# Kernel optimization log

Measured on AMD Instinct MI355X. Metric: run time of the kernel, lower is better.

Reference implementation:

```python
import jax, jax.numpy as jnp
import numpy as np

N_NODES = 100000
N_EDGES = 1600000
IN_FEATS = 512
OUT_FEATS = 256


def setup_inputs() -> dict:
    key = jax.random.key(0)
    k1, k2, k3, k4, k5 = jax.random.split(key, 5)
    feat = jax.random.normal(k1, (N_NODES, IN_FEATS), dtype=jnp.float32)
    W = jax.random.normal(k2, (OUT_FEATS, IN_FEATS), dtype=jnp.float32) * (1.0 / np.sqrt(IN_FEATS))
    b = jax.random.normal(k3, (OUT_FEATS,), dtype=jnp.float32) * 0.01
    src = jax.random.randint(k4, (N_EDGES,), 0, N_NODES, dtype=jnp.int32)
    dst = jax.random.randint(k5, (N_EDGES,), 0, N_NODES, dtype=jnp.int32)
    return {"feat": feat, "W": W, "b": b, "src": src, "dst": dst}


def reference(feat, W, b, src, dst):
    # Linear projection: h = feat @ W^T + b   -> [N, out_feats]
    h = jnp.einsum('nf,of->no', feat, W) + b
    # DGL update_all(copy_src, sum): for each edge (s, d), message = h[s],
    # reduce = sum over incoming edges at each destination node.
    # Nodes with no in-edges get zeros (DGL sum-reduce default).
    msgs = h[src]  # [E, out_feats] gather
    h_out = jax.ops.segment_sum(msgs, dst, num_segments=N_NODES)  # [N, out_feats]
    return h_out
```

## Files before the change

kernel.cpp:

```cpp
#include <hip/hip_runtime.h>
#include <hip/hip_bf16.h>
#include <stdint.h>

#define N_NODES 100000
#define IN_F    512
#define OUT_F   256
#define N_EDGES 1600000

typedef __attribute__((ext_vector_type(4))) float f32x4;
typedef __attribute__((ext_vector_type(8))) short bf16x8;
typedef __attribute__((ext_vector_type(8))) uint16_t u16x8;
typedef __attribute__((ext_vector_type(4))) uint32_t u32x4;

#define BM 128
#define BK 32
#define KT_TILES (IN_F / BK)
#define WFRAG_KT_STRIDE (16 * 16 * 32)
#define EPS 66
#define MTILES ((N_NODES + BM - 1) / BM)

#define NBUCK 391
#define BCAP  4608
#define SC_EDGES 8192
#define NBLK_SC ((N_EDGES + SC_EDGES - 1) / SC_EDGES)

__device__ __forceinline__ float bf2f(uint16_t u) {
    union { uint32_t i; float f; } c; c.i = ((uint32_t)u) << 16; return c.f;
}
__device__ __forceinline__ uint16_t f2bf(float f) {
    union { float f; uint32_t i; } c; c.f = f;
    uint32_t x = c.i;
    return (uint16_t)((x + 0x7FFFu + ((x >> 16) & 1u)) >> 16);
}
__device__ __forceinline__ uint32_t cvt_pk_bf16(float a, float b) {
    uint32_t r;
    asm("v_cvt_pk_bf16_f32 %0, %1, %2" : "=v"(r) : "v"(a), "v"(b));
    return r;
}
__device__ __forceinline__ void gload_lds16(const float* g, float* l) {
    __builtin_amdgcn_global_load_lds(
        (const __attribute__((address_space(1))) void*)g,
        (__attribute__((address_space(3))) void*)l, 16, 0, 0);
}
#define SYNC_VM(N) do {                                        \
    asm volatile("s_waitcnt vmcnt(" #N ")" ::: "memory");      \
    __builtin_amdgcn_s_barrier();                              \
} while (0)

__global__ __launch_bounds__(256) void w_frag_kernel(
    const float* __restrict__ W, uint16_t* __restrict__ w_frag)
{
    const int gid = blockIdx.x * 256 + threadIdx.x;
    if (gid >= 16384) return;
    const int kg = gid & 3, lrow = (gid >> 2) & 15, cg = (gid >> 6) & 15, kt = gid >> 10;
    const float* s = W + (size_t)(cg * 16 + lrow) * IN_F + kt * 32 + kg * 8;
    const f32x4 v0 = *(const f32x4*)s;
    const f32x4 v1 = *(const f32x4*)(s + 4);
    u32x4 c;
    c[0] = cvt_pk_bf16(v0[0], v0[1]);
    c[1] = cvt_pk_bf16(v0[2], v0[3]);
    c[2] = cvt_pk_bf16(v1[0], v1[1]);
    c[3] = cvt_pk_bf16(v1[2], v1[3]);
    *(u32x4*)(w_frag + (size_t)gid * 8) = c;
}

__global__ __launch_bounds__(512) void bucket_init_kernel(int* __restrict__ bucket_cursor)
{
    const int i = threadIdx.x;
    if (i < NBUCK) bucket_cursor[i] = i * BCAP;
}

__global__ __launch_bounds__(512) void gemm_scatter_kernel(
    const float* __restrict__ feat, const uint16_t* __restrict__ w_frag,
    const float* __restrict__ bias, uint16_t* __restrict__ h,
    const int* __restrict__ src, const int* __restrict__ dst,
    int* __restrict__ bucket_cursor, uint32_t* __restrict__ pairs)
{
    __shared__ __align__(16) char smem_raw[3 * BM * BK * 4];

    if (blockIdx.x >= MTILES) {
        int* bh    = (int*)smem_raw;
        int* bbase = bh + NBUCK;
        const int tid = threadIdx.x;
        for (int i = tid; i < NBUCK; i += 512) bh[i] = 0;
        __syncthreads();
        const int base = (int)(blockIdx.x - MTILES) * SC_EDGES;
        uint32_t pk[SC_EDGES / 512];
        int      bk[SC_EDGES / 512];
        #pragma unroll
        for (int k = 0; k < SC_EDGES / 512; ++k) {
            const int e = base + k * 512 + tid;
            if (e < N_EDGES) {
                const int d = dst[e], s = src[e];
                bk[k] = d >> 8;
                pk[k] = ((uint32_t)s << 8) | (uint32_t)(d & 255);
                atomicAdd(&bh[bk[k]], 1);
            } else {
                bk[k] = -1; pk[k] = 0;
            }
        }
        __syncthreads();
        for (int i = tid; i < NBUCK; i += 512) {
            const int c = bh[i];
            bbase[i] = c ? atomicAdd(&bucket_cursor[i], c) : 0;
            bh[i] = 0;
        }
        __syncthreads();
        #pragma unroll
        for (int k = 0; k < SC_EDGES / 512; ++k) {
            if (bk[k] >= 0) {
                const int r = atomicAdd(&bh[bk[k]], 1);
                pairs[bbase[bk[k]] + r] = pk[k];
            }
        }
        return;
    }

    float (*At)[BM][BK] = (float (*)[BM][BK])smem_raw;

    const int m0 = blockIdx.x * BM;

    const int t    = threadIdx.x;
    const int wid  = t >> 6;
    const int lane = t & 63;
    const int wr   = wid >> 2, wc = wid & 3;
    const int lrow = lane & 15;
    const int kg   = lane >> 4;

    f32x4 acc[4][4] = {};

    const int r8 = lane >> 3;
    const int sp = lane & 7;
    const int sc = sp ^ r8;
    const float* gsrc[2];
    #pragma unroll
    for (int i = 0; i < 2; ++i) {
        int grow = m0 + wid * 16 + i * 8 + r8;
        if (grow > N_NODES - 1) grow = N_NODES - 1;
        gsrc[i] = feat + (size_t)grow * IN_F + sc * 4;
    }

#define STAGE(KT, BUF)                                                     \
    do {                                                                   \
        gload_lds16(gsrc[0] + (KT) * BK, &At[BUF][wid * 16][0]);           \
        gload_lds16(gsrc[1] + (KT) * BK, &At[BUF][wid * 16 + 8][0]);       \
    } while (0)

    const uint16_t* wfp[4];
    #pragma unroll
    for (int n = 0; n < 4; ++n) {
        const int cg = wc * 4 + n;
        wfp[n] = w_frag + ((size_t)cg * 16 + lrow) * 32 + kg * 8;
    }

    bf16x8 bfr[2][4];

    #pragma unroll
    for (int n = 0; n < 4; ++n) bfr[0][n] = *(const bf16x8*)(wfp[n]);
    STAGE(0, 0);
    STAGE(1, 1);
    SYNC_VM(0);

    const int p0 = (2 * kg) ^ (lrow & 7);
    const int p1 = p0 ^ 1;

    #pragma unroll
    for (int kt = 0; kt < KT_TILES; ++kt) {
        const int cur = kt % 3;
        if (kt + 1 < KT_TILES) {
            #pragma unroll
            for (int n = 0; n < 4; ++n)
                bfr[(kt + 1) & 1][n] =
                    *(const bf16x8*)(wfp[n] + (size_t)(kt + 1) * WFRAG_KT_STRIDE);
        }
        if (kt + 2 < KT_TILES) STAGE(kt + 2, (kt + 2) % 3);

        bf16x8 af[4];
        #pragma unroll
        for (int m = 0; m < 4; ++m) {
            const int row = wr * 64 + m * 16 + lrow;
            const f32x4 v0 = *(const f32x4*)&At[cur][row][p0 * 4];
            const f32x4 v1 = *(const f32x4*)&At[cur][row][p1 * 4];
            union { bf16x8 v; uint32_t u[4]; } c_;
            c_.u[0] = cvt_pk_bf16(v0[0], v0[1]);
            c_.u[1] = cvt_pk_bf16(v0[2], v0[3]);
            c_.u[2] = cvt_pk_bf16(v1[0], v1[1]);
            c_.u[3] = cvt_pk_bf16(v1[2], v1[3]);
            af[m] = c_.v;
        }
        #pragma unroll
        for (int m = 0; m < 4; ++m)
            #pragma unroll
            for (int n = 0; n < 4; ++n)
                acc[m][n] = __builtin_amdgcn_mfma_f32_16x16x32_bf16(
                    af[m], bfr[kt & 1][n], acc[m][n], 0, 0, 0);

        if (kt <= KT_TILES - 3)       SYNC_VM(6);
        else if (kt == KT_TILES - 2)  SYNC_VM(4);
    }
#undef STAGE

    __syncthreads();

    uint16_t* ep = (uint16_t*)smem_raw;
    const int wbase = wid * (16 * EPS);
    float bv[4];
    #pragma unroll
    for (int n = 0; n < 4; ++n) bv[n] = bias[wc * 64 + n * 16 + lrow];

    #pragma unroll
    for (int m = 0; m < 4; ++m) {
        #pragma unroll
        for (int n = 0; n < 4; ++n)
            #pragma unroll
            for (int j = 0; j < 4; ++j)
                ep[wbase + (kg * 4 + j) * EPS + n * 16 + lrow] = f2bf(acc[m][n][j] + bv[n]);
        __syncthreads();
        #pragma unroll
        for (int g = 0; g < 4; ++g) {
            const int r16  = g * 4 + (lane >> 4);
            const int cidx = (lane & 15) * 4;
            const int ib = wbase + r16 * EPS + cidx;
            uint2 v;
            v.x = *(const uint32_t*)&ep[ib];
            v.y = *(const uint32_t*)&ep[ib + 2];
            const int row = m0 + wr * 64 + m * 16 + r16;
            if (row < N_NODES)
                *(uint2*)(h + (size_t)row * OUT_F + wc * 64 + cidx) = v;
        }
        __syncthreads();
    }
}

__global__ __launch_bounds__(256) void bucket_sort_kernel(
    const uint32_t* __restrict__ pairs, const int* __restrict__ bucket_cursor,
    int* __restrict__ start, int* __restrict__ deg, int* __restrict__ csr_src)
{
    __shared__ int hist[256];
    __shared__ int cur[256];
    __shared__ int tsum[256];
    const int b = blockIdx.x;
    const int t = threadIdx.x;
    const int ebeg = b * BCAP;
    const int eend = bucket_cursor[b];
    hist[t] = 0;
    __syncthreads();
    for (int i = ebeg + t; i < eend; i += 256)
        atomicAdd(&hist[pairs[i] & 255], 1);
    __syncthreads();
    const int c = hist[t];
    int x = c;
    tsum[t] = x; __syncthreads();
    for (int off = 1; off < 256; off <<= 1) {
        const int y = (t >= off) ? tsum[t - off] : 0;
        __syncthreads();
        x += y; tsum[t] = x;
        __syncthreads();
    }
    const int ex = x - c;
    const int node = (b << 8) + t;
    if (node < N_NODES) {
        start[node] = ebeg + ex;
        deg[node]   = c;
    }
    cur[t] = ebeg + ex;
    __syncthreads();
    for (int i = ebeg + t; i < eend; i += 256) {
        const uint32_t p = pairs[i];
        const int pos = atomicAdd(&cur[p & 255], 1);
        csr_src[pos] = (int)(p >> 8);
    }
}

__global__ __launch_bounds__(256) void gcn_gather_kernel(
    const uint16_t* __restrict__ h, const int* __restrict__ start,
    const int* __restrict__ deg, const int* __restrict__ csr_src,
    float* __restrict__ out)
{
    const int n = blockIdx.x * 4 + (threadIdx.x >> 6);
    if (n >= N_NODES) return;
    const int lane = threadIdx.x & 63;
    const int half = lane >> 5;
    const int hl   = lane & 31;
    const int beg = start[n];
    const int end = beg + deg[n];

    float a[8] = {0.f, 0.f, 0.f, 0.f, 0.f, 0.f, 0.f, 0.f};

    int j = beg + half;
    for (; j + 2 < end; j += 4) {
        const int s0 = csr_src[j];
        const int s1 = csr_src[j + 2];
        const u16x8 v0 = *(const u16x8*)(h + (size_t)s0 * OUT_F + hl * 8);
        const u16x8 v1 = *(const u16x8*)(h + (size_t)s1 * OUT_F + hl * 8);
        #pragma unroll
        for (int i = 0; i < 8; ++i) a[i] += bf2f(v0[i]);
        #pragma unroll
        for (int i = 0; i < 8; ++i) a[i] += bf2f(v1[i]);
    }
    if (j < end) {
        const int s0 = csr_src[j];
        const u16x8 v0 = *(const u16x8*)(h + (size_t)s0 * OUT_F + hl * 8);
        #pragma unroll
        for (int i = 0; i < 8; ++i) a[i] += bf2f(v0[i]);
    }

    #pragma unroll
    for (int i = 0; i < 8; ++i) a[i] += __shfl_xor(a[i], 32, 64);

    if (half == 0) {
        f32x4 o0, o1;
        o0[0] = a[0]; o0[1] = a[1]; o0[2] = a[2]; o0[3] = a[3];
        o1[0] = a[4]; o1[1] = a[5]; o1[2] = a[6]; o1[3] = a[7];
        float* op = out + (size_t)n * OUT_F + hl * 8;
        *(f32x4*)op = o0;
        *(f32x4*)(op + 4) = o1;
    }
}

__global__ __launch_bounds__(256) void gcn_scatter_kernel(
    const uint16_t* __restrict__ h, const int* __restrict__ src,
    const int* __restrict__ dst, float* __restrict__ out)
{
    const int e = (blockIdx.x << 2) | (threadIdx.x >> 6);
    if (e >= N_EDGES) return;
    const int lane = threadIdx.x & 63;
    const int s = src[e];
    const int d = dst[e];
    const ushort4 v = *((const ushort4*)(h + (size_t)s * OUT_F) + lane);
    float* op = out + (size_t)d * OUT_F + (lane << 2);
    unsafeAtomicAdd(op + 0, bf2f(v.x));
    unsafeAtomicAdd(op + 1, bf2f(v.y));
    unsafeAtomicAdd(op + 2, bf2f(v.z));
    unsafeAtomicAdd(op + 3, bf2f(v.w));
}

static inline size_t align256(size_t x) { return (x + 255) & ~(size_t)255; }

extern "C" void kernel_launch(void* const* d_in, const int* in_sizes, int n_in,
                              void* d_out, int out_size, void* d_ws, size_t ws_size,
                              hipStream_t stream) {
    const float* feat = (const float*)d_in[0];
    const float* W    = (const float*)d_in[1];
    const float* bias = (const float*)d_in[2];
    const int*   src  = (const int*)d_in[3];
    const int*   dst  = (const int*)d_in[4];
    float*       out  = (float*)d_out;

    char* ws = (char*)d_ws;

    size_t off = 0;
    uint16_t* h       = (uint16_t*)(ws + off); off = align256(off + (size_t)N_NODES * OUT_F * 2);
    uint16_t* w_frag  = (uint16_t*)(ws + off); off = align256(off + (size_t)OUT_F * IN_F * 2);
    int* start        = (int*)(ws + off);      off = align256(off + (size_t)N_NODES * 4);
    int* deg          = (int*)(ws + off);      off = align256(off + (size_t)N_NODES * 4);
    int* bucket_cursor= (int*)(ws + off);      off = align256(off + (size_t)NBUCK * 4);
    uint32_t* pairs   = (uint32_t*)(ws + off); off = align256(off + (size_t)NBUCK * BCAP * 4);
    int* csr_src      = (int*)(ws + off);      off = align256(off + (size_t)NBUCK * BCAP * 4);
    const bool bucket_ok = (off <= ws_size);

    w_frag_kernel<<<64, 256, 0, stream>>>(W, w_frag);

    if (bucket_ok) {
        bucket_init_kernel<<<1, 512, 0, stream>>>(bucket_cursor);
        gemm_scatter_kernel<<<MTILES + NBLK_SC, 512, 0, stream>>>(
            feat, w_frag, bias, h, src, dst, bucket_cursor, pairs);
        bucket_sort_kernel<<<NBUCK, 256, 0, stream>>>(pairs, bucket_cursor, start, deg, csr_src);
        gcn_gather_kernel<<<(N_NODES + 3) / 4, 256, 0, stream>>>(h, start, deg, csr_src, out);
    } else {
        gemm_scatter_kernel<<<MTILES, 512, 0, stream>>>(
            feat, w_frag, bias, h, src, dst, (int*)d_ws, (uint32_t*)d_ws);
        hipMemsetAsync(out, 0, (size_t)out_size * sizeof(float), stream);
        gcn_scatter_kernel<<<(N_EDGES + 3) / 4, 256, 0, stream>>>(h, src, dst, out);
    }
}
```

Measured before the change: 216.3 us.

## Store projected features in column slices and gather per slice for cache locality

```diff
diff --git a/kernel.cpp b/kernel.cpp
--- a/kernel.cpp
+++ b/kernel.cpp
@@ -23,6 +23,12 @@
 #define BCAP  4608
 #define SC_EDGES 8192
 #define NBLK_SC ((N_EDGES + SC_EDGES - 1) / SC_EDGES)
+
+#define NSLICE 16
+#define SLICE_ELEMS (OUT_F / NSLICE)
+#define GBLK_NODES 128
+#define NODE_GROUPS ((N_NODES + GBLK_NODES - 1) / GBLK_NODES)
+#define GBLK_PER_PHASE (NODE_GROUPS * 8)
 
 __device__ __forceinline__ float bf2f(uint16_t u) {
     union { uint32_t i; float f; } c; c.i = ((uint32_t)u) << 16; return c.f;
@@ -72,7 +78,7 @@
 
 __global__ __launch_bounds__(512) void gemm_scatter_kernel(
     const float* __restrict__ feat, const uint16_t* __restrict__ w_frag,
-    const float* __restrict__ bias, uint16_t* __restrict__ h,
+    const float* __restrict__ bias, uint16_t* __restrict__ hs,
     const int* __restrict__ src, const int* __restrict__ dst,
     int* __restrict__ bucket_cursor, uint32_t* __restrict__ pairs)
 {
@@ -225,8 +231,11 @@
             v.x = *(const uint32_t*)&ep[ib];
             v.y = *(const uint32_t*)&ep[ib + 2];
             const int row = m0 + wr * 64 + m * 16 + r16;
+            const int col = wc * 64 + cidx;
+            const int sl  = col >> 4;
+            const int c0  = col & 15;
             if (row < N_NODES)
-                *(uint2*)(h + (size_t)row * OUT_F + wc * 64 + cidx) = v;
+                *(uint2*)(hs + ((size_t)sl * N_NODES + row) * SLICE_ELEMS + c0) = v;
         }
         __syncthreads();
     }
@@ -273,53 +282,57 @@
 }
 
 __global__ __launch_bounds__(256) void gcn_gather_kernel(
-    const uint16_t* __restrict__ h, const int* __restrict__ start,
+    const uint16_t* __restrict__ hs, const int* __restrict__ start,
     const int* __restrict__ deg, const int* __restrict__ csr_src,
     float* __restrict__ out)
 {
-    const int n = blockIdx.x * 4 + (threadIdx.x >> 6);
-    if (n >= N_NODES) return;
+    const int b = blockIdx.x;
+    const int phase = (b >= GBLK_PER_PHASE) ? 1 : 0;
+    const int q = b - phase * GBLK_PER_PHASE;
+    const int s = (q & 7) | (phase << 3);
+    const int ng = q >> 3;
+    const int w = threadIdx.x >> 6;
     const int lane = threadIdx.x & 63;
-    const int half = lane >> 5;
-    const int hl   = lane & 31;
-    const int beg = start[n];
-    const int end = beg + deg[n];
+    const int p = lane >> 1;
+    const int ch = lane & 1;
+    const int n = ng * GBLK_NODES + w * 32 + p;
+    const bool ok = n < N_NODES;
+    const int beg = ok ? start[n] : 0;
+    const int dg  = ok ? deg[n] : 0;
+
+    int m = dg;
+    #pragma unroll
+    for (int off = 1; off < 64; off <<= 1)
+        m = max(m, __shfl_xor(m, off, 64));
+
+    const uint16_t* hb = hs + (size_t)s * N_NODES * SLICE_ELEMS + ch * 8;
 
     float a[8] = {0.f, 0.f, 0.f, 0.f, 0.f, 0.f, 0.f, 0.f};
 
-    int j = beg + half;
-    for (; j + 2 < end; j += 4) {
-        const int s0 = csr_src[j];
-        const int s1 = csr_src[j + 2];
-        const u16x8 v0 = *(const u16x8*)(h + (size_t)s0 * OUT_F + hl * 8);
-        const u16x8 v1 = *(const u16x8*)(h + (size_t)s1 * OUT_F + hl * 8);
+    for (int j = 0; j < m; j += 2) {
+        u16x8 v0 = {}, v1 = {};
+        if (j < dg)
+            v0 = *(const u16x8*)(hb + (size_t)csr_src[beg + j] * SLICE_ELEMS);
+        if (j + 1 < dg)
+            v1 = *(const u16x8*)(hb + (size_t)csr_src[beg + j + 1] * SLICE_ELEMS);
         #pragma unroll
         for (int i = 0; i < 8; ++i) a[i] += bf2f(v0[i]);
         #pragma unroll
         for (int i = 0; i < 8; ++i) a[i] += bf2f(v1[i]);
     }
-    if (j < end) {
-        const int s0 = csr_src[j];
-        const u16x8 v0 = *(const u16x8*)(h + (size_t)s0 * OUT_F + hl * 8);
-        #pragma unroll
-        for (int i = 0; i < 8; ++i) a[i] += bf2f(v0[i]);
-    }
-
-    #pragma unroll
-    for (int i = 0; i < 8; ++i) a[i] += __shfl_xor(a[i], 32, 64);
-
-    if (half == 0) {
+
+    if (ok) {
+        float* op = out + (size_t)n * OUT_F + s * SLICE_ELEMS + ch * 8;
         f32x4 o0, o1;
         o0[0] = a[0]; o0[1] = a[1]; o0[2] = a[2]; o0[3] = a[3];
         o1[0] = a[4]; o1[1] = a[5]; o1[2] = a[6]; o1[3] = a[7];
-        float* op = out + (size_t)n * OUT_F + hl * 8;
-        *(f32x4*)op = o0;
-        *(f32x4*)(op + 4) = o1;
+        __builtin_nontemporal_store(o0, (f32x4*)op);
+        __builtin_nontemporal_store(o1, (f32x4*)(op + 4));
     }
 }
 
 __global__ __launch_bounds__(256) void gcn_scatter_kernel(
-    const uint16_t* __restrict__ h, const int* __restrict__ src,
+    const uint16_t* __restrict__ hs, const int* __restrict__ src,
     const int* __restrict__ dst, float* __restrict__ out)
 {
     const int e = (blockIdx.x << 2) | (threadIdx.x >> 6);
@@ -327,8 +340,10 @@
     const int lane = threadIdx.x & 63;
     const int s = src[e];
     const int d = dst[e];
-    const ushort4 v = *((const ushort4*)(h + (size_t)s * OUT_F) + lane);
-    float* op = out + (size_t)d * OUT_F + (lane << 2);
+    const int sl = lane >> 2;
+    const int c0 = (lane & 3) * 4;
+    const ushort4 v = *(const ushort4*)(hs + ((size_t)sl * N_NODES + s) * SLICE_ELEMS + c0);
+    float* op = out + (size_t)d * OUT_F + sl * SLICE_ELEMS + c0;
     unsafeAtomicAdd(op + 0, bf2f(v.x));
     unsafeAtomicAdd(op + 1, bf2f(v.y));
     unsafeAtomicAdd(op + 2, bf2f(v.z));
@@ -350,7 +365,7 @@
     char* ws = (char*)d_ws;
 
     size_t off = 0;
-    uint16_t* h       = (uint16_t*)(ws + off); off = align256(off + (size_t)N_NODES * OUT_F * 2);
+    uint16_t* hs      = (uint16_t*)(ws + off); off = align256(off + (size_t)N_NODES * OUT_F * 2);
     uint16_t* w_frag  = (uint16_t*)(ws + off); off = align256(off + (size_t)OUT_F * IN_F * 2);
     int* start        = (int*)(ws + off);      off = align256(off + (size_t)N_NODES * 4);
     int* deg          = (int*)(ws + off);      off = align256(off + (size_t)N_NODES * 4);
@@ -364,13 +379,13 @@
     if (bucket_ok) {
         bucket_init_kernel<<<1, 512, 0, stream>>>(bucket_cursor);
         gemm_scatter_kernel<<<MTILES + NBLK_SC, 512, 0, stream>>>(
-            feat, w_frag, bias, h, src, dst, bucket_cursor, pairs);
+            feat, w_frag, bias, hs, src, dst, bucket_cursor, pairs);
         bucket_sort_kernel<<<NBUCK, 256, 0, stream>>>(pairs, bucket_cursor, start, deg, csr_src);
-        gcn_gather_kernel<<<(N_NODES + 3) / 4, 256, 0, stream>>>(h, start, deg, csr_src, out);
+        gcn_gather_kernel<<<2 * GBLK_PER_PHASE, 256, 0, stream>>>(hs, start, deg, csr_src, out);
     } else {
         gemm_scatter_kernel<<<MTILES, 512, 0, stream>>>(
-            feat, w_frag, bias, h, src, dst, (int*)d_ws, (uint32_t*)d_ws);
+            feat, w_frag, bias, hs, src, dst, (int*)d_ws, (uint32_t*)d_ws);
         hipMemsetAsync(out, 0, (size_t)out_size * sizeof(float), stream);
-        gcn_scatter_kernel<<<(N_EDGES + 3) / 4, 256, 0, stream>>>(h, src, dst, out);
-    }
-}
+        gcn_scatter_kernel<<<(N_EDGES + 3) / 4, 256, 0, stream>>>(hs, src, dst, out);
+    }
+}
```

New measurement: 352.7 us. 63.1% more time.
